# Optimization experiments

Hardware: AMD Instinct MI355X
Metric: run time of the kernel (lower is better)

Reference implementation:

```python
import jax, jax.numpy as jnp
import numpy as np

KB = 0.0019872041      # Boltzmann constant, kcal/(mol*K)
TEMP = 300.0
ALPHA = 10.0
BW = 0.15              # Gaussian KDE bandwidth
PAIR_I = jnp.array([0, 0, 0, 1, 1, 2])
PAIR_J = jnp.array([1, 2, 3, 2, 3, 3])

B, N_ATOMS = 512, 1024
G, L, K, D = 256, 8, 128, 6


def setup_inputs() -> dict:
    key = jax.random.key(0)
    k1, k2, k3, k4, k5, k6 = jax.random.split(key, 6)
    positions = jax.random.normal(k1, (B, N_ATOMS, 3), dtype=jnp.float32) * 2.0
    # KDE training samples live in 6-dim distance space (positive, few Angstroms)
    kde_samples = jax.random.uniform(k2, (G, L, K, D), dtype=jnp.float32) * 5.0
    weight = jax.random.uniform(k3, (G, L), dtype=jnp.float32)
    offset = jax.random.normal(k4, (G, L), dtype=jnp.float32)
    atom_idxs = jax.random.randint(k5, (G, L, 4), 0, N_ATOMS)
    group_sizes = jax.random.randint(k6, (G,), 0, L)  # clamped to >=1 in reference
    return {"positions": positions, "kde_samples": kde_samples, "weight": weight,
            "offset": offset, "atom_idxs": atom_idxs, "group_sizes": group_sizes}


def reference(positions, kde_samples, weight, offset, atom_idxs, group_sizes):
    Gn, Ln, Kn, Dn = kde_samples.shape
    # Gather the 4 vertices of every loss: [B, G, L, 4, 3]
    vp = positions[:, atom_idxs]
    # 6 pairwise distances per loss: [B, G, L, 6]
    diff = vp[..., PAIR_I, :] - vp[..., PAIR_J, :]
    dists = jnp.sqrt(jnp.sum(diff * diff, axis=-1) + 1e-12)
    # Gaussian KDE log-density over the K training samples, expanded squared
    x2 = jnp.sum(dists * dists, axis=-1)          # [B,G,L]
    mu2 = jnp.sum(kde_samples * kde_samples, -1)  # [G,L,K]
    xmu = jnp.einsum('bgld,glkd->bglk', dists, kde_samples)
    sq = x2[..., None] + mu2[None] - 2.0 * xmu    # [B,G,L,K]
    log_norm = jnp.log(jnp.float32(Kn)) + 0.5 * Dn * jnp.log(2.0 * jnp.pi * BW * BW)
    logP = jax.nn.logsumexp(-sq / (2.0 * BW * BW), axis=-1) - log_norm  # [B,G,L]
    energy = -KB * TEMP * logP
    scaled = energy * weight + offset             # [B,G,L]
    # Ragged group reduction: min over the valid losses of each group
    sizes = jnp.maximum(group_sizes, 1)
    mask = jnp.arange(Ln)[None, :] < sizes[:, None]        # [G,L]
    group_min = jnp.min(jnp.where(mask, scaled, jnp.inf), axis=-1)  # [B,G]
    # soft-min across groups
    return -jax.nn.logsumexp(-ALPHA * group_min, axis=-1) / ALPHA   # [B]
```

## Files before the change

### kernel.cpp

```cpp
#include <hip/hip_runtime.h>

#define NB 512
#define NATOMS 1024
#define NG 256
#define NL 8
#define NK 128

#define KBT 0.59616123f
#define ALPHA_C 10.0f
#define LN2 0.6931471805599453f
#define LOG2E 1.4426950408889634f
#define INV2BW2 22.222221f
#define SCALE2 (INV2BW2 * LOG2E)
#define LOG_NORM (-1.0170649f)

#define WL_CAP 2048
#define FILL_BLOCKS 128

typedef _Float16 f16x8 __attribute__((ext_vector_type(8)));
typedef float f32x16 __attribute__((ext_vector_type(16)));

__device__ __forceinline__ float fexp2(float x) { return __builtin_amdgcn_exp2f(x); }
__device__ __forceinline__ float flog2(float x) { return __builtin_amdgcn_logf(x); }

__device__ __forceinline__ unsigned fkey(float f) {
  unsigned u = __float_as_uint(f);
  return (u & 0x80000000u) ? ~u : (u | 0x80000000u);
}
__device__ __forceinline__ float funkey(unsigned k) {
  unsigned u = (k & 0x80000000u) ? (k ^ 0x80000000u) : ~k;
  return __uint_as_float(u);
}

__device__ __forceinline__ float wred_min(float v) {
#pragma unroll
  for (int m = 32; m >= 1; m >>= 1) v = fminf(v, __shfl_xor(v, m, 64));
  return v;
}
__device__ __forceinline__ float wred_sum(float v) {
#pragma unroll
  for (int m = 32; m >= 1; m >>= 1) v += __shfl_xor(v, m, 64);
  return v;
}

__global__ __launch_bounds__(256) void prep_small(
    const int* __restrict__ gsizes, int* __restrict__ wl,
    uint4* __restrict__ gmin_u4) {
  const int t = threadIdx.x;
  if (blockIdx.x != 0) {
    const unsigned F = 0xFFFFFFFFu;
    gmin_u4[(blockIdx.x - 1) * 256 + t] = make_uint4(F, F, F, F);
    return;
  }
  const int lane = t & 63, wid = t >> 6;
  int gs = gsizes[t];
  int nl = gs < 1 ? 1 : (gs > NL ? NL : gs);
  int x = nl;
#pragma unroll
  for (int m = 1; m < 64; m <<= 1) {
    int y = __shfl_up(x, m, 64);
    if (lane >= m) x += y;
  }
  __shared__ int wsum[4];
  if (lane == 63) wsum[wid] = x;
  __syncthreads();
  int off = 0;
  for (int i = 0; i < wid; ++i) off += wsum[i];
  int inc = off + x, exc = inc - nl;
  for (int j = 0; j < nl; ++j) wl[exc + j] = (t << 3) | j;
  if (t == 255) wl[WL_CAP] = inc;
}

__global__ __launch_bounds__(256) void stage1_kernel(
    const float* __restrict__ positions, const float* __restrict__ kde,
    const float* __restrict__ weight, const float* __restrict__ offs,
    const int* __restrict__ atom_idxs, const int* __restrict__ wl,
    unsigned* __restrict__ gmin_u) {
  const int count = wl[WL_CAP];
  const int w = blockIdx.x;
  if (w >= count) return;
  const int gl = wl[w];
  const int g = gl >> 3;

  const int t = threadIdx.x;
  const int lane = t & 63;
  const int wid = t >> 6;
  const int col = lane & 31, h = lane >> 5;

  __shared__ f16x8 tabL[8][64];

  const int4 idx = *reinterpret_cast<const int4*>(atom_idxs + (gl << 2));
  const int ids[4] = {idx.x, idx.y, idx.z, idx.w};

  float px[2][4], py[2][4], pz[2][4];
  {
    const int b = (wid << 5) + col;
    const float* pb = positions + (size_t)b * NATOMS * 3;
#pragma unroll
    for (int j = 0; j < 4; ++j) {
      const float3 p = *reinterpret_cast<const float3*>(pb + ids[j] * 3);
      px[0][j] = p.x; py[0][j] = p.y; pz[0][j] = p.z;
    }
  }

  if (t < NK) {
    const float* mp = kde + ((size_t)gl * NK + t) * 6;
    float mu2 = 0.0f;
    _Float16 ah[6], al[6];
#pragma unroll
    for (int q = 0; q < 6; ++q) {
      float mv = mp[q];
      mu2 += mv * mv;
      float a = (2.0f * SCALE2) * mv;
      _Float16 hh = (_Float16)a;
      ah[q] = hh;
      al[q] = (_Float16)(a - (float)hh);
    }
    float z = -SCALE2 * mu2;
    _Float16 z1 = (_Float16)z;
    _Float16 z2 = (_Float16)(z - (float)z1);
    const _Float16 Z = (_Float16)0.0f;
    const int kt = t >> 5, m = t & 31;
    tabL[kt * 2 + 0][m]      = (f16x8){ah[0],ah[1],ah[2],ah[3],ah[4],ah[5],al[0],al[1]};
    tabL[kt * 2 + 0][m + 32] = (f16x8){al[2],al[3],al[4],al[5],ah[0],ah[1],ah[2],ah[3]};
    tabL[kt * 2 + 1][m]      = (f16x8){ah[4],ah[5],al[0],al[1],al[2],al[3],al[4],al[5]};
    tabL[kt * 2 + 1][m + 32] = (f16x8){z1,  z2,  Z,   Z,   Z,   Z,   Z,   Z   };
  }
  __syncthreads();

  const float wgt = weight[gl], off = offs[gl];
  const int PI_[6] = {0, 0, 0, 1, 1, 2};
  const int PJ_[6] = {1, 2, 3, 2, 3, 3};
  const _Float16 ONE = (_Float16)1.0f, Z = (_Float16)0.0f;
  const f32x16 zz = {0.0f};

#pragma unroll
  for (int gg = 0; gg < 4; ++gg) {
    const int cur = gg & 1;
    if (gg < 3) {
      const int bn = ((gg + 1) << 7) + (wid << 5) + col;
      const float* pb = positions + (size_t)bn * NATOMS * 3;
#pragma unroll
      for (int j = 0; j < 4; ++j) {
        const float3 p = *reinterpret_cast<const float3*>(pb + ids[j] * 3);
        px[cur ^ 1][j] = p.x; py[cur ^ 1][j] = p.y; pz[cur ^ 1][j] = p.z;
      }
    }
    const int b = (gg << 7) + (wid << 5) + col;

    float d[6]; float x2 = 0.0f;
#pragma unroll
    for (int q = 0; q < 6; ++q) {
      float dx = px[cur][PI_[q]] - px[cur][PJ_[q]];
      float dy = py[cur][PI_[q]] - py[cur][PJ_[q]];
      float dz = pz[cur][PI_[q]] - pz[cur][PJ_[q]];
      float dd = dx * dx + dy * dy + dz * dz + 1e-12f;
      d[q] = sqrtf(dd);
      x2 += d[q] * d[q];
    }
    const float c2 = -x2 * SCALE2;

    _Float16 xh[6], xl[6];
#pragma unroll
    for (int q = 0; q < 6; ++q) {
      _Float16 hh = (_Float16)d[q];
      xh[q] = hh;
      xl[q] = (_Float16)(d[q] - (float)hh);
    }
    f16x8 Bf0 = (h == 0)
      ? (f16x8){xh[0],xh[1],xh[2],xh[3],xh[4],xh[5],xh[0],xh[1]}
      : (f16x8){xh[2],xh[3],xh[4],xh[5],xl[0],xl[1],xl[2],xl[3]};
    f16x8 Bf1 = (h == 0)
      ? (f16x8){xl[4],xl[5],xl[0],xl[1],xl[2],xl[3],xl[4],xl[5]}
      : (f16x8){ONE,  ONE,  Z,   Z,   Z,   Z,   Z,   Z   };

    f32x16 acc[4];
#pragma unroll
    for (int kt = 0; kt < 4; ++kt) {
      f16x8 A0 = tabL[kt * 2 + 0][lane];
      f16x8 A1 = tabL[kt * 2 + 1][lane];
      acc[kt] = __builtin_amdgcn_mfma_f32_32x32x16_f16(
          A1, Bf1, __builtin_amdgcn_mfma_f32_32x32x16_f16(A0, Bf0, zz, 0, 0, 0),
          0, 0, 0);
    }

    float mkt[4];
#pragma unroll
    for (int kt = 0; kt < 4; ++kt) {
      float m0 = fmaxf(fmaxf(acc[kt][0], acc[kt][1]), fmaxf(acc[kt][2], acc[kt][3]));
      float m1 = fmaxf(fmaxf(acc[kt][4], acc[kt][5]), fmaxf(acc[kt][6], acc[kt][7]));
      float m2 = fmaxf(fmaxf(acc[kt][8], acc[kt][9]), fmaxf(acc[kt][10], acc[kt][11]));
      float m3 = fmaxf(fmaxf(acc[kt][12], acc[kt][13]), fmaxf(acc[kt][14], acc[kt][15]));
      mkt[kt] = fmaxf(fmaxf(m0, m1), fmaxf(m2, m3));
    }
    float mx = fmaxf(fmaxf(mkt[0], mkt[1]), fmaxf(mkt[2], mkt[3]));
    mx = fmaxf(mx, __shfl_xor(mx, 32, 64));

    float s0 = 0.0f, s1 = 0.0f, s2 = 0.0f, s3 = 0.0f;
#pragma unroll
    for (int kt = 0; kt < 4; ++kt) {
      s0 += fexp2(acc[kt][0] - mx)  + fexp2(acc[kt][1] - mx)
          + fexp2(acc[kt][2] - mx)  + fexp2(acc[kt][3] - mx);
      s1 += fexp2(acc[kt][4] - mx)  + fexp2(acc[kt][5] - mx)
          + fexp2(acc[kt][6] - mx)  + fexp2(acc[kt][7] - mx);
      s2 += fexp2(acc[kt][8] - mx)  + fexp2(acc[kt][9] - mx)
          + fexp2(acc[kt][10] - mx) + fexp2(acc[kt][11] - mx);
      s3 += fexp2(acc[kt][12] - mx) + fexp2(acc[kt][13] - mx)
          + fexp2(acc[kt][14] - mx) + fexp2(acc[kt][15] - mx);
    }
    float s = (s0 + s1) + (s2 + s3);
    s += __shfl_xor(s, 32, 64);

    if (h == 0) {
      float lse2 = c2 + mx + flog2(s);
      float logP = lse2 * LN2 - LOG_NORM;
      float scaled = -KBT * logP * wgt + off;
      atomicMin(&gmin_u[g * NB + b], fkey(scaled));
    }
  }
}

__global__ __launch_bounds__(256) void stage2_kernel(
    const unsigned* __restrict__ gmin_u, float* __restrict__ out) {
  const int b = blockIdx.x;
  const int t = threadIdx.x;
  const int lane = t & 63;
  const int wid = t >> 6;
  float v = funkey(gmin_u[t * NB + b]);
  __shared__ float sm[4], ss[4];
  float m = wred_min(v);
  if (lane == 0) sm[wid] = m;
  __syncthreads();
  float M = fminf(fminf(sm[0], sm[1]), fminf(sm[2], sm[3]));
  float e = fexp2(-ALPHA_C * LOG2E * (v - M));
  float s = wred_sum(e);
  if (lane == 0) ss[wid] = s;
  __syncthreads();
  if (t == 0) {
    float S = ss[0] + ss[1] + ss[2] + ss[3];
    out[b] = M - flog2(S) * LN2 / ALPHA_C;
  }
}

extern "C" void kernel_launch(void* const* d_in, const int* in_sizes, int n_in,
                              void* d_out, int out_size, void* d_ws, size_t ws_size,
                              hipStream_t stream) {
  const float* positions = (const float*)d_in[0];
  const float* kde       = (const float*)d_in[1];
  const float* weight    = (const float*)d_in[2];
  const float* offs      = (const float*)d_in[3];
  const int*   atom_idxs = (const int*)d_in[4];
  const int*   gsizes    = (const int*)d_in[5];
  float* out = (float*)d_out;

  unsigned* gmin_u = (unsigned*)d_ws;
  int* wl = (int*)d_ws + (size_t)NG * NB;

  prep_small<<<dim3(1 + FILL_BLOCKS), dim3(256), 0, stream>>>(
      gsizes, wl, (uint4*)gmin_u);
  stage1_kernel<<<dim3(WL_CAP), dim3(256), 0, stream>>>(
      positions, kde, weight, offs, atom_idxs, wl, gmin_u);
  stage2_kernel<<<dim3(NB), dim3(256), 0, stream>>>(gmin_u, out);
}
```

Before: 37.73 us.

## Replace atomicMin group reduction with per-loss stores and per-wave KDE tables

Stage 1 now writes each loss's scaled energy to a [G*L, B] buffer instead of doing atomicMin into a pre-filled group buffer. The ragged min over losses moves into stage 2, which also drops the fill blocks from the prep kernel. Each wave builds its own copy of the KDE A-operand table in LDS, which removes the block-wide __syncthreads. The batch mapping changes so each wave handles a contiguous range of 128 batch rows. The cost is redundant table construction in every wave, four times the LDS use, and a larger intermediate buffer that stage 2 reads with strided loads.

```diff
diff --git a/kernel.cpp b/kernel.cpp
--- a/kernel.cpp
+++ b/kernel.cpp
@@ -15,7 +15,6 @@
 #define LOG_NORM (-1.0170649f)
 
 #define WL_CAP 2048
-#define FILL_BLOCKS 128
 
 typedef _Float16 f16x8 __attribute__((ext_vector_type(8)));
 typedef float f32x16 __attribute__((ext_vector_type(16)));
@@ -23,15 +22,6 @@
 __device__ __forceinline__ float fexp2(float x) { return __builtin_amdgcn_exp2f(x); }
 __device__ __forceinline__ float flog2(float x) { return __builtin_amdgcn_logf(x); }
 
-__device__ __forceinline__ unsigned fkey(float f) {
-  unsigned u = __float_as_uint(f);
-  return (u & 0x80000000u) ? ~u : (u | 0x80000000u);
-}
-__device__ __forceinline__ float funkey(unsigned k) {
-  unsigned u = (k & 0x80000000u) ? (k ^ 0x80000000u) : ~k;
-  return __uint_as_float(u);
-}
-
 __device__ __forceinline__ float wred_min(float v) {
 #pragma unroll
   for (int m = 32; m >= 1; m >>= 1) v = fminf(v, __shfl_xor(v, m, 64));
@@ -43,15 +33,9 @@
   return v;
 }
 
-__global__ __launch_bounds__(256) void prep_small(
-    const int* __restrict__ gsizes, int* __restrict__ wl,
-    uint4* __restrict__ gmin_u4) {
+__global__ __launch_bounds__(256) void prep_wl(
+    const int* __restrict__ gsizes, int* __restrict__ wl) {
   const int t = threadIdx.x;
-  if (blockIdx.x != 0) {
-    const unsigned F = 0xFFFFFFFFu;
-    gmin_u4[(blockIdx.x - 1) * 256 + t] = make_uint4(F, F, F, F);
-    return;
-  }
   const int lane = t & 63, wid = t >> 6;
   int gs = gsizes[t];
   int nl = gs < 1 ? 1 : (gs > NL ? NL : gs);
@@ -75,26 +59,25 @@
     const float* __restrict__ positions, const float* __restrict__ kde,
     const float* __restrict__ weight, const float* __restrict__ offs,
     const int* __restrict__ atom_idxs, const int* __restrict__ wl,
-    unsigned* __restrict__ gmin_u) {
+    float* __restrict__ scaled_out) {
   const int count = wl[WL_CAP];
   const int w = blockIdx.x;
   if (w >= count) return;
   const int gl = wl[w];
-  const int g = gl >> 3;
 
   const int t = threadIdx.x;
   const int lane = t & 63;
   const int wid = t >> 6;
   const int col = lane & 31, h = lane >> 5;
 
-  __shared__ f16x8 tabL[8][64];
+  __shared__ f16x8 tabL[4][8][64];
 
   const int4 idx = *reinterpret_cast<const int4*>(atom_idxs + (gl << 2));
   const int ids[4] = {idx.x, idx.y, idx.z, idx.w};
 
   float px[2][4], py[2][4], pz[2][4];
   {
-    const int b = (wid << 5) + col;
+    const int b = (wid << 7) + col;
     const float* pb = positions + (size_t)b * NATOMS * 3;
 #pragma unroll
     for (int j = 0; j < 4; ++j) {
@@ -103,8 +86,10 @@
     }
   }
 
-  if (t < NK) {
-    const float* mp = kde + ((size_t)gl * NK + t) * 6;
+#pragma unroll
+  for (int r = 0; r < 2; ++r) {
+    const int k = lane + (r << 6);
+    const float* mp = kde + ((size_t)gl * NK + k) * 6;
     float mu2 = 0.0f;
     _Float16 ah[6], al[6];
 #pragma unroll
@@ -120,13 +105,12 @@
     _Float16 z1 = (_Float16)z;
     _Float16 z2 = (_Float16)(z - (float)z1);
     const _Float16 Z = (_Float16)0.0f;
-    const int kt = t >> 5, m = t & 31;
-    tabL[kt * 2 + 0][m]      = (f16x8){ah[0],ah[1],ah[2],ah[3],ah[4],ah[5],al[0],al[1]};
-    tabL[kt * 2 + 0][m + 32] = (f16x8){al[2],al[3],al[4],al[5],ah[0],ah[1],ah[2],ah[3]};
-    tabL[kt * 2 + 1][m]      = (f16x8){ah[4],ah[5],al[0],al[1],al[2],al[3],al[4],al[5]};
-    tabL[kt * 2 + 1][m + 32] = (f16x8){z1,  z2,  Z,   Z,   Z,   Z,   Z,   Z   };
-  }
-  __syncthreads();
+    const int kt = k >> 5, m = k & 31;
+    tabL[wid][kt * 2 + 0][m]      = (f16x8){ah[0],ah[1],ah[2],ah[3],ah[4],ah[5],al[0],al[1]};
+    tabL[wid][kt * 2 + 0][m + 32] = (f16x8){al[2],al[3],al[4],al[5],ah[0],ah[1],ah[2],ah[3]};
+    tabL[wid][kt * 2 + 1][m]      = (f16x8){ah[4],ah[5],al[0],al[1],al[2],al[3],al[4],al[5]};
+    tabL[wid][kt * 2 + 1][m + 32] = (f16x8){z1,  z2,  Z,   Z,   Z,   Z,   Z,   Z   };
+  }
 
   const float wgt = weight[gl], off = offs[gl];
   const int PI_[6] = {0, 0, 0, 1, 1, 2};
@@ -138,7 +122,7 @@
   for (int gg = 0; gg < 4; ++gg) {
     const int cur = gg & 1;
     if (gg < 3) {
-      const int bn = ((gg + 1) << 7) + (wid << 5) + col;
+      const int bn = (wid << 7) + ((gg + 1) << 5) + col;
       const float* pb = positions + (size_t)bn * NATOMS * 3;
 #pragma unroll
       for (int j = 0; j < 4; ++j) {
@@ -146,7 +130,7 @@
         px[cur ^ 1][j] = p.x; py[cur ^ 1][j] = p.y; pz[cur ^ 1][j] = p.z;
       }
     }
-    const int b = (gg << 7) + (wid << 5) + col;
+    const int b = (wid << 7) + (gg << 5) + col;
 
     float d[6]; float x2 = 0.0f;
 #pragma unroll
@@ -177,8 +161,8 @@
     f32x16 acc[4];
 #pragma unroll
     for (int kt = 0; kt < 4; ++kt) {
-      f16x8 A0 = tabL[kt * 2 + 0][lane];
-      f16x8 A1 = tabL[kt * 2 + 1][lane];
+      f16x8 A0 = tabL[wid][kt * 2 + 0][lane];
+      f16x8 A1 = tabL[wid][kt * 2 + 1][lane];
       acc[kt] = __builtin_amdgcn_mfma_f32_32x32x16_f16(
           A1, Bf1, __builtin_amdgcn_mfma_f32_32x32x16_f16(A0, Bf0, zz, 0, 0, 0),
           0, 0, 0);
@@ -214,19 +198,25 @@
     if (h == 0) {
       float lse2 = c2 + mx + flog2(s);
       float logP = lse2 * LN2 - LOG_NORM;
-      float scaled = -KBT * logP * wgt + off;
-      atomicMin(&gmin_u[g * NB + b], fkey(scaled));
+      float sc = -KBT * logP * wgt + off;
+      scaled_out[(size_t)gl * NB + b] = sc;
     }
   }
 }
 
 __global__ __launch_bounds__(256) void stage2_kernel(
-    const unsigned* __restrict__ gmin_u, float* __restrict__ out) {
+    const float* __restrict__ scaled_in, const int* __restrict__ gsizes,
+    float* __restrict__ out) {
   const int b = blockIdx.x;
   const int t = threadIdx.x;
   const int lane = t & 63;
   const int wid = t >> 6;
-  float v = funkey(gmin_u[t * NB + b]);
+  int gs = gsizes[t];
+  int nl = gs < 1 ? 1 : (gs > NL ? NL : gs);
+  float v = 1e30f;
+  for (int l = 0; l < nl; ++l)
+    v = fminf(v, scaled_in[(size_t)((t << 3) + l) * NB + b]);
+
   __shared__ float sm[4], ss[4];
   float m = wred_min(v);
   if (lane == 0) sm[wid] = m;
@@ -253,12 +243,11 @@
   const int*   gsizes    = (const int*)d_in[5];
   float* out = (float*)d_out;
 
-  unsigned* gmin_u = (unsigned*)d_ws;
-  int* wl = (int*)d_ws + (size_t)NG * NB;
-
-  prep_small<<<dim3(1 + FILL_BLOCKS), dim3(256), 0, stream>>>(
-      gsizes, wl, (uint4*)gmin_u);
+  float* scaled = (float*)d_ws;
+  int* wl = (int*)((char*)d_ws + (4 << 20));
+
+  prep_wl<<<dim3(1), dim3(256), 0, stream>>>(gsizes, wl);
   stage1_kernel<<<dim3(WL_CAP), dim3(256), 0, stream>>>(
-      positions, kde, weight, offs, atom_idxs, wl, gmin_u);
-  stage2_kernel<<<dim3(NB), dim3(256), 0, stream>>>(gmin_u, out);
-}
+      positions, kde, weight, offs, atom_idxs, wl, scaled);
+  stage2_kernel<<<dim3(NB), dim3(256), 0, stream>>>(scaled, gsizes, out);
+}
```

After: 39.18 us. +3.8%, slower.
